# Optimization experiments

Hardware: AMD Instinct MI355X
Metric: run time of the kernel (lower is better)

Reference implementation:

```python
import jax, jax.numpy as jnp
import numpy as np

B, S, D, H = 4, 2048, 1024, 16
DK = D // H
NEG = -1e9


def setup_inputs() -> dict:
    key = jax.random.key(0)
    k1, k2, k3, k4 = jax.random.split(key, 4)
    x = jax.random.normal(k1, (B, S, D), dtype=jnp.float32)
    # seq_lens sorted descending; first entry must equal max_len (as the torch
    # code uses seq_lens[0] as max_len for the mask)
    sl = jax.random.randint(k2, (B,), S // 2, S + 1)
    sl = jnp.sort(sl)[::-1].at[0].set(S).astype(jnp.int64)
    # params of the output projection nn.Linear(d_m, d_m)
    lim = 1.0 / np.sqrt(D)
    W = jax.random.uniform(k3, (D, D), minval=-lim, maxval=lim, dtype=jnp.float32)
    b = jax.random.uniform(k4, (D,), minval=-lim, maxval=lim, dtype=jnp.float32)
    return {"x": x, "seq_lens": sl, "W": W, "b": b}


def reference(x, seq_lens, W, b):
    # key padding mask: (B, 1, 1, S) -> True where key position is valid
    valid = jnp.arange(S)[None, :] < seq_lens[:, None]          # (B, S)
    mask = valid[:, None, None, :]                              # (B, 1, 1, S)
    # split heads: (B, S, D) -> (B, H, S, DK)
    xh = x.reshape(B, S, H, DK).transpose(0, 2, 1, 3)
    scores = jnp.einsum("bhqd,bhkd->bhqk", xh, xh) / jnp.sqrt(jnp.float32(DK))
    scores = jnp.where(mask, scores, NEG)
    attn = jax.nn.softmax(scores, axis=-1)                      # (B, H, S, S)
    # dropout(0.1) omitted (eval-mode deterministic reference)
    ctx = jnp.einsum("bhqk,bhkd->bhqd", attn, xh)
    ctx = ctx.transpose(0, 2, 1, 3).reshape(B, S, D)
    out = ctx @ W.T + b                                         # (B, S, D)
    return (jnp.sum(out, axis=1), attn)
```

## Files before the change

kernel.cpp:

```cpp
#include <hip/hip_runtime.h>

#define S_  2048
#define D_  1024
#define H_  16
#define B_  4
#define NT  32

typedef __attribute__((ext_vector_type(8))) short short8;
typedef __attribute__((ext_vector_type(4))) float f32x4;

__device__ __forceinline__ unsigned short f2bf(float f) {
  unsigned int u = __float_as_uint(f);
  u += 0x7fffu + ((u >> 16) & 1u);
  return (unsigned short)(u >> 16);
}
__device__ __forceinline__ unsigned int pack2(float a, float b) {
  return (unsigned int)f2bf(a) | ((unsigned int)f2bf(b) << 16);
}
__device__ __forceinline__ float h2f(unsigned int u, int shft) {
  unsigned short hs = (unsigned short)(u >> shft);
  return (float)__builtin_bit_cast(_Float16, hs);
}

#define SCL   0.18033688011112042f
#define EBIAS 12.0f

__global__ __launch_bounds__(256) void xcvt(const float* __restrict__ x,
                                            unsigned short* __restrict__ xh) {
  const int n = blockIdx.x;
  const int bh = n >> 5, chunk = n & 31;
  const int b = bh >> 4, h = bh & 15;
  const int r = threadIdx.x >> 2, cg = threadIdx.x & 3;
  const int srow = chunk * 64 + r;
  const float* src = x + ((size_t)b * S_ + srow) * D_ + h * 64 + cg * 16;
  float4 v0 = ((const float4*)src)[0];
  float4 v1 = ((const float4*)src)[1];
  float4 v2 = ((const float4*)src)[2];
  float4 v3 = ((const float4*)src)[3];
  uint4 w0, w1;
  w0.x = pack2(v0.x, v0.y); w0.y = pack2(v0.z, v0.w);
  w0.z = pack2(v1.x, v1.y); w0.w = pack2(v1.z, v1.w);
  w1.x = pack2(v2.x, v2.y); w1.y = pack2(v2.z, v2.w);
  w1.z = pack2(v3.x, v3.y); w1.w = pack2(v3.z, v3.w);
  unsigned short* dst = xh + ((size_t)bh * S_ + srow) * 64 + cg * 16;
  *(uint4*)dst = w0;
  *(uint4*)(dst + 8) = w1;
}

__global__ __launch_bounds__(768, 1) void attn_fused(
    const unsigned short* __restrict__ xh, const int* __restrict__ sl32,
    float* __restrict__ attn, unsigned int* __restrict__ cpart)
{
  __shared__ __align__(16) unsigned int ebuf[2][8][2048];
  __shared__ float wbuf[128];
  __shared__ float invbuf[2][16];

  const int n    = blockIdx.x;
  const int xcd  = n & 7;
  const int j    = n >> 3;
  const int bh   = (j >> 2) * 8 + xcd;
  const int q0   = (j & 3) * NT;
  const int b    = bh >> 4;
  const int tid  = threadIdx.x;
  const int wv   = tid >> 6;
  const bool is_comp = wv < 8;
  const int lane = tid & 63;
  const int lo   = lane & 15;
  const int g    = lane >> 4;

  const bool is64 = (sl32[1] == 0);
  const int seqlen = is64 ? sl32[2 * b] : sl32[b];

  const unsigned short* xk = xh + (size_t)bh * S_ * 64;

  const int sA = ((g * 2) & 6) << 2;
  const int wt  = tid & 255;
  const int wr  = wt >> 4, wc = wt & 15;
  const int r2w = wr >> 1, shw = (wr & 1) * 16, sw2 = (r2w & 6) << 2;

  for (int ti = 0; ti <= NT; ++ti) {
    unsigned int (*eb)[2048] = ebuf[ti & 1];
    const unsigned int (*ebp)[2048] = ebuf[(ti + 1) & 1];

    if (is_comp) {
      if (ti < NT) {
        const int qt = q0 + ti;
        short8 aq0 = *(const short8*)(xk + (size_t)(qt * 16 + lo) * 64 + g * 8);
        short8 aq1 = *(const short8*)(xk + (size_t)(qt * 16 + lo) * 64 + g * 8 + 32);
        float r0 = 0.f, r1 = 0.f, r2s = 0.f, r3 = 0.f;
#pragma unroll 4
        for (int c = 0; c < 16; ++c) {
          const int kt = c * 8 + wv;
          const int kg = kt * 16 + lo;
          const unsigned short* kp = xk + (size_t)kg * 64 + g * 8;
          short8 b0 = *(const short8*)kp;
          short8 b1 = *(const short8*)(kp + 32);
          f32x4 acc = {0.f, 0.f, 0.f, 0.f};
          acc = __builtin_amdgcn_mfma_f32_16x16x32_bf16(aq0, b0, acc, 0, 0, 0);
          acc = __builtin_amdgcn_mfma_f32_16x16x32_bf16(aq1, b1, acc, 0, 0, 0);
          const bool valid = kg < seqlen;
          float e0 = valid ? exp2f(acc[0] * SCL - EBIAS) : 0.f;
          float e1 = valid ? exp2f(acc[1] * SCL - EBIAS) : 0.f;
          float e2 = valid ? exp2f(acc[2] * SCL - EBIAS) : 0.f;
          float e3 = valid ? exp2f(acc[3] * SCL - EBIAS) : 0.f;
          r0 += e0; r1 += e1; r2s += e2; r3 += e3;
          eb[g * 2][kg ^ sA] =
              __builtin_bit_cast(unsigned int, __builtin_amdgcn_cvt_pkrtz(e0, e1));
          eb[g * 2 + 1][kg ^ sA] =
              __builtin_bit_cast(unsigned int, __builtin_amdgcn_cvt_pkrtz(e2, e3));
        }
        float rs[4] = {r0, r1, r2s, r3};
#pragma unroll
        for (int r4 = 0; r4 < 4; ++r4) {
          float v = rs[r4];
          v += __shfl_xor(v, 1);
          v += __shfl_xor(v, 2);
          v += __shfl_xor(v, 4);
          v += __shfl_xor(v, 8);
          if (lo == 0) wbuf[wv * 16 + g * 4 + r4] = v;
        }
      }
    } else if (ti > 0) {
      const float* ivp = invbuf[(ti - 1) & 1];
      const float vr = ivp[wr];
      float* prow = attn + (size_t)bh * S_ * S_ +
                    (size_t)((q0 + ti - 1) * 16 + wr) * S_;
#pragma unroll 8
      for (int i = 0; i < 32; ++i) {
        const int k0 = wc * 4 + i * 64;
        uint4 u = *(const uint4*)&ebp[r2w][k0 ^ sw2];
        f32x4 v = {h2f(u.x, shw) * vr, h2f(u.y, shw) * vr,
                   h2f(u.z, shw) * vr, h2f(u.w, shw) * vr};
        __builtin_nontemporal_store(v, (f32x4*)(prow + k0));
      }
      const int c0 = wt * 8;
      float a0 = 0.f, a1 = 0.f, a2 = 0.f, a3 = 0.f;
      float a4 = 0.f, a5 = 0.f, a6 = 0.f, a7 = 0.f;
#pragma unroll
      for (int r2 = 0; r2 < 8; ++r2) {
        const int s = (r2 & 6) << 2;
        const uint4 uA = *(const uint4*)&ebp[r2][c0 ^ s];
        const uint4 uB = *(const uint4*)&ebp[r2][(c0 ^ s) + 4];
        const float i0 = ivp[2 * r2], i1 = ivp[2 * r2 + 1];
        a0 += h2f(uA.x, 0) * i0 + h2f(uA.x, 16) * i1;
        a1 += h2f(uA.y, 0) * i0 + h2f(uA.y, 16) * i1;
        a2 += h2f(uA.z, 0) * i0 + h2f(uA.z, 16) * i1;
        a3 += h2f(uA.w, 0) * i0 + h2f(uA.w, 16) * i1;
        a4 += h2f(uB.x, 0) * i0 + h2f(uB.x, 16) * i1;
        a5 += h2f(uB.y, 0) * i0 + h2f(uB.y, 16) * i1;
        a6 += h2f(uB.z, 0) * i0 + h2f(uB.z, 16) * i1;
        a7 += h2f(uB.w, 0) * i0 + h2f(uB.w, 16) * i1;
      }
      uint4 w;
      w.x = __builtin_bit_cast(unsigned int, __builtin_amdgcn_cvt_pkrtz(a0, a1));
      w.y = __builtin_bit_cast(unsigned int, __builtin_amdgcn_cvt_pkrtz(a2, a3));
      w.z = __builtin_bit_cast(unsigned int, __builtin_amdgcn_cvt_pkrtz(a4, a5));
      w.w = __builtin_bit_cast(unsigned int, __builtin_amdgcn_cvt_pkrtz(a6, a7));
      *(uint4*)&cpart[(size_t)(bh * 128 + q0 + ti - 1) * 1024 + wt * 4] = w;
    }

    __syncthreads();
    if (ti < NT && tid < 16) {
      float s = 0.f;
#pragma unroll
      for (int w8 = 0; w8 < 8; ++w8) s += wbuf[w8 * 16 + tid];
      invbuf[ti & 1][tid] = 1.0f / s;
    }
    __syncthreads();
  }
}

__global__ __launch_bounds__(256) void csum2(const unsigned int* __restrict__ cpart,
                                             const unsigned short* __restrict__ xh,
                                             float* __restrict__ csump) {
  __shared__ float csh[256];
  __shared__ float part[4][64];
  const int bh = blockIdx.x >> 3, oct = blockIdx.x & 7;
  const int t = threadIdx.x;
  {
    const int k = oct * 256 + t;
    const unsigned short* cp =
        (const unsigned short*)cpart + (size_t)bh * 128 * 2048 + k;
    float s = 0.f;
#pragma unroll 8
    for (int q = 0; q < 128; ++q)
      s += (float)__builtin_bit_cast(_Float16, cp[(size_t)q * 2048]);
    csh[t] = s;
  }
  __syncthreads();
  const int seg = t >> 6, d = t & 63;
  const unsigned short* xb = xh + (size_t)bh * S_ * 64 + d;
  const int k0 = oct * 256 + seg * 64;
  float acc = 0.f;
#pragma unroll 4
  for (int kk = 0; kk < 64; ++kk) {
    float xv = __uint_as_float((unsigned int)xb[(size_t)(k0 + kk) * 64] << 16);
    acc += csh[seg * 64 + kk] * xv;
  }
  part[seg][d] = acc;
  __syncthreads();
  if (t < 64)
    csump[((size_t)oct * 64 + bh) * 64 + d] =
        part[0][d] + part[1][d] + part[2][d] + part[3][d];
}

__global__ __launch_bounds__(256) void proj_k(const float* __restrict__ csump,
                                              const float* __restrict__ W,
                                              const float* __restrict__ bias,
                                              float* __restrict__ out0) {
  const int idx = blockIdx.x * 4 + (threadIdx.x >> 6);
  const int b = idx >> 10, d = idx & 1023;
  const int lane = threadIdx.x & 63;
  const float* wr = W + (size_t)d * D_;
  float acc = 0.f;
#pragma unroll
  for (int e = 0; e < 16; ++e) {
    const int ei = lane + e * 64;
    const int bhh = b * 16 + (ei >> 6);
    const int dd = ei & 63;
    float cv = 0.f;
#pragma unroll
    for (int oct = 0; oct < 8; ++oct)
      cv += csump[((size_t)oct * 64 + bhh) * 64 + dd];
    acc += cv * wr[ei];
  }
  acc += __shfl_xor(acc, 32);
  acc += __shfl_xor(acc, 16);
  acc += __shfl_xor(acc, 8);
  acc += __shfl_xor(acc, 4);
  acc += __shfl_xor(acc, 2);
  acc += __shfl_xor(acc, 1);
  if (lane == 0) out0[idx] = acc + 2048.0f * bias[d];
}

extern "C" void kernel_launch(void* const* d_in, const int* in_sizes, int n_in,
                              void* d_out, int out_size, void* d_ws, size_t ws_size,
                              hipStream_t stream) {
  const float* x    = (const float*)d_in[0];
  const int*   sl   = (const int*)d_in[1];
  const float* W    = (const float*)d_in[2];
  const float* bias = (const float*)d_in[3];

  float* out0 = (float*)d_out;
  float* attn = out0 + B_ * D_;

  unsigned int* cpart = (unsigned int*)d_ws;
  float* csump = (float*)(cpart + (size_t)64 * 128 * 1024);
  unsigned short* xh = (unsigned short*)(csump + 8 * 64 * 64);

  hipLaunchKernelGGL(xcvt,       dim3(2048), dim3(256), 0, stream, x, xh);
  hipLaunchKernelGGL(attn_fused, dim3(256),  dim3(768), 0, stream, xh, sl, attn, cpart);
  hipLaunchKernelGGL(csum2,      dim3(512),  dim3(256), 0, stream, cpart, xh, csump);
  hipLaunchKernelGGL(proj_k,     dim3(1024), dim3(256), 0, stream, csump, W, bias, out0);
}
```

Baseline: 352.7 us.

## Merge compute and writer warp roles into unified 512-thread interleaved loop

The fused attention kernel drops its split of 8 compute waves plus 4 writer waves and uses 8 waves that each do both jobs. In the same loop, each wave interleaves the MFMA/exp work for the current query tile with the normalized attn stores for the previous tile. The column-partial reduction now runs right after the inverse sums are ready, reading the current buffer rather than waiting a step. Barriers are replaced by an explicit lgkmcnt wait plus s_barrier. The aim is to spread the large attn store stream across more waves and let it overlap with compute, at the cost of heavier per-wave register and instruction pressure.

```diff
diff --git a/kernel.cpp b/kernel.cpp
--- a/kernel.cpp
+++ b/kernel.cpp
@@ -20,6 +20,11 @@
 __device__ __forceinline__ float h2f(unsigned int u, int shft) {
   unsigned short hs = (unsigned short)(u >> shft);
   return (float)__builtin_bit_cast(_Float16, hs);
+}
+
+__device__ __forceinline__ void bar_lgkm() {
+  asm volatile("s_waitcnt lgkmcnt(0)" ::: "memory");
+  __builtin_amdgcn_s_barrier();
 }
 
 #define SCL   0.18033688011112042f
@@ -47,7 +52,7 @@
   *(uint4*)(dst + 8) = w1;
 }
 
-__global__ __launch_bounds__(768, 1) void attn_fused(
+__global__ __launch_bounds__(512, 1) void attn_fused(
     const unsigned short* __restrict__ xh, const int* __restrict__ sl32,
     float* __restrict__ attn, unsigned int* __restrict__ cpart)
 {
@@ -63,7 +68,6 @@
   const int b    = bh >> 4;
   const int tid  = threadIdx.x;
   const int wv   = tid >> 6;
-  const bool is_comp = wv < 8;
   const int lane = tid & 63;
   const int lo   = lane & 15;
   const int g    = lane >> 4;
@@ -74,99 +78,97 @@
   const unsigned short* xk = xh + (size_t)bh * S_ * 64;
 
   const int sA = ((g * 2) & 6) << 2;
-  const int wt  = tid & 255;
-  const int wr  = wt >> 4, wc = wt & 15;
-  const int r2w = wr >> 1, shw = (wr & 1) * 16, sw2 = (r2w & 6) << 2;
+  const int row_w = tid >> 5;
+  const int cu    = tid & 31;
+  const int r2w = row_w >> 1, shw = (row_w & 1) * 16, sw2 = (r2w & 6) << 2;
+  const int c0 = tid * 4;
 
   for (int ti = 0; ti <= NT; ++ti) {
     unsigned int (*eb)[2048] = ebuf[ti & 1];
     const unsigned int (*ebp)[2048] = ebuf[(ti + 1) & 1];
-
-    if (is_comp) {
-      if (ti < NT) {
-        const int qt = q0 + ti;
-        short8 aq0 = *(const short8*)(xk + (size_t)(qt * 16 + lo) * 64 + g * 8);
-        short8 aq1 = *(const short8*)(xk + (size_t)(qt * 16 + lo) * 64 + g * 8 + 32);
-        float r0 = 0.f, r1 = 0.f, r2s = 0.f, r3 = 0.f;
-#pragma unroll 4
-        for (int c = 0; c < 16; ++c) {
-          const int kt = c * 8 + wv;
-          const int kg = kt * 16 + lo;
-          const unsigned short* kp = xk + (size_t)kg * 64 + g * 8;
-          short8 b0 = *(const short8*)kp;
-          short8 b1 = *(const short8*)(kp + 32);
-          f32x4 acc = {0.f, 0.f, 0.f, 0.f};
-          acc = __builtin_amdgcn_mfma_f32_16x16x32_bf16(aq0, b0, acc, 0, 0, 0);
-          acc = __builtin_amdgcn_mfma_f32_16x16x32_bf16(aq1, b1, acc, 0, 0, 0);
-          const bool valid = kg < seqlen;
-          float e0 = valid ? exp2f(acc[0] * SCL - EBIAS) : 0.f;
-          float e1 = valid ? exp2f(acc[1] * SCL - EBIAS) : 0.f;
-          float e2 = valid ? exp2f(acc[2] * SCL - EBIAS) : 0.f;
-          float e3 = valid ? exp2f(acc[3] * SCL - EBIAS) : 0.f;
-          r0 += e0; r1 += e1; r2s += e2; r3 += e3;
-          eb[g * 2][kg ^ sA] =
-              __builtin_bit_cast(unsigned int, __builtin_amdgcn_cvt_pkrtz(e0, e1));
-          eb[g * 2 + 1][kg ^ sA] =
-              __builtin_bit_cast(unsigned int, __builtin_amdgcn_cvt_pkrtz(e2, e3));
-        }
-        float rs[4] = {r0, r1, r2s, r3};
-#pragma unroll
-        for (int r4 = 0; r4 < 4; ++r4) {
-          float v = rs[r4];
-          v += __shfl_xor(v, 1);
-          v += __shfl_xor(v, 2);
-          v += __shfl_xor(v, 4);
-          v += __shfl_xor(v, 8);
-          if (lo == 0) wbuf[wv * 16 + g * 4 + r4] = v;
-        }
-      }
-    } else if (ti > 0) {
-      const float* ivp = invbuf[(ti - 1) & 1];
-      const float vr = ivp[wr];
-      float* prow = attn + (size_t)bh * S_ * S_ +
-                    (size_t)((q0 + ti - 1) * 16 + wr) * S_;
-#pragma unroll 8
-      for (int i = 0; i < 32; ++i) {
-        const int k0 = wc * 4 + i * 64;
-        uint4 u = *(const uint4*)&ebp[r2w][k0 ^ sw2];
+    const bool has_c = ti < NT;
+    const bool has_w = ti > 0;
+
+    short8 aq0 = {}, aq1 = {};
+    if (has_c) {
+      const int qt = q0 + ti;
+      aq0 = *(const short8*)(xk + (size_t)(qt * 16 + lo) * 64 + g * 8);
+      aq1 = *(const short8*)(xk + (size_t)(qt * 16 + lo) * 64 + g * 8 + 32);
+    }
+    float r0 = 0.f, r1 = 0.f, r2s = 0.f, r3 = 0.f;
+    const float vr = has_w ? invbuf[(ti + 1) & 1][row_w] : 0.f;
+    float* prow = attn + (size_t)bh * S_ * S_ +
+                  (size_t)((q0 + ti - 1) * 16 + row_w) * S_;
+
+#pragma unroll
+    for (int i = 0; i < 16; ++i) {
+      if (has_c) {
+        const int kt = i * 8 + wv;
+        const int kg = kt * 16 + lo;
+        const unsigned short* kp = xk + (size_t)kg * 64 + g * 8;
+        short8 b0 = *(const short8*)kp;
+        short8 b1 = *(const short8*)(kp + 32);
+        f32x4 acc = {0.f, 0.f, 0.f, 0.f};
+        acc = __builtin_amdgcn_mfma_f32_16x16x32_bf16(aq0, b0, acc, 0, 0, 0);
+        acc = __builtin_amdgcn_mfma_f32_16x16x32_bf16(aq1, b1, acc, 0, 0, 0);
+        const bool valid = kg < seqlen;
+        float e0 = valid ? exp2f(acc[0] * SCL - EBIAS) : 0.f;
+        float e1 = valid ? exp2f(acc[1] * SCL - EBIAS) : 0.f;
+        float e2 = valid ? exp2f(acc[2] * SCL - EBIAS) : 0.f;
+        float e3 = valid ? exp2f(acc[3] * SCL - EBIAS) : 0.f;
+        r0 += e0; r1 += e1; r2s += e2; r3 += e3;
+        eb[g * 2][kg ^ sA] =
+            __builtin_bit_cast(unsigned int, __builtin_amdgcn_cvt_pkrtz(e0, e1));
+        eb[g * 2 + 1][kg ^ sA] =
+            __builtin_bit_cast(unsigned int, __builtin_amdgcn_cvt_pkrtz(e2, e3));
+      }
+      if (has_w) {
+        const int col0 = i * 128 + cu * 4;
+        uint4 u = *(const uint4*)&ebp[r2w][col0 ^ sw2];
         f32x4 v = {h2f(u.x, shw) * vr, h2f(u.y, shw) * vr,
                    h2f(u.z, shw) * vr, h2f(u.w, shw) * vr};
-        __builtin_nontemporal_store(v, (f32x4*)(prow + k0));
-      }
-      const int c0 = wt * 8;
+        __builtin_nontemporal_store(v, (f32x4*)(prow + col0));
+      }
+    }
+
+    if (has_c) {
+      float rs[4] = {r0, r1, r2s, r3};
+#pragma unroll
+      for (int r4 = 0; r4 < 4; ++r4) {
+        float v = rs[r4];
+        v += __shfl_xor(v, 1);
+        v += __shfl_xor(v, 2);
+        v += __shfl_xor(v, 4);
+        v += __shfl_xor(v, 8);
+        if (lo == 0) wbuf[wv * 16 + g * 4 + r4] = v;
+      }
+    }
+    bar_lgkm();
+    if (has_c && tid < 16) {
+      float s = 0.f;
+#pragma unroll
+      for (int w8 = 0; w8 < 8; ++w8) s += wbuf[w8 * 16 + tid];
+      invbuf[ti & 1][tid] = 1.0f / s;
+    }
+    bar_lgkm();
+    if (has_c) {
+      const float* ivc = invbuf[ti & 1];
       float a0 = 0.f, a1 = 0.f, a2 = 0.f, a3 = 0.f;
-      float a4 = 0.f, a5 = 0.f, a6 = 0.f, a7 = 0.f;
 #pragma unroll
       for (int r2 = 0; r2 < 8; ++r2) {
         const int s = (r2 & 6) << 2;
-        const uint4 uA = *(const uint4*)&ebp[r2][c0 ^ s];
-        const uint4 uB = *(const uint4*)&ebp[r2][(c0 ^ s) + 4];
-        const float i0 = ivp[2 * r2], i1 = ivp[2 * r2 + 1];
-        a0 += h2f(uA.x, 0) * i0 + h2f(uA.x, 16) * i1;
-        a1 += h2f(uA.y, 0) * i0 + h2f(uA.y, 16) * i1;
-        a2 += h2f(uA.z, 0) * i0 + h2f(uA.z, 16) * i1;
-        a3 += h2f(uA.w, 0) * i0 + h2f(uA.w, 16) * i1;
-        a4 += h2f(uB.x, 0) * i0 + h2f(uB.x, 16) * i1;
-        a5 += h2f(uB.y, 0) * i0 + h2f(uB.y, 16) * i1;
-        a6 += h2f(uB.z, 0) * i0 + h2f(uB.z, 16) * i1;
-        a7 += h2f(uB.w, 0) * i0 + h2f(uB.w, 16) * i1;
-      }
-      uint4 w;
+        const uint4 u = *(const uint4*)&eb[r2][c0 ^ s];
+        const float i0 = ivc[2 * r2], i1 = ivc[2 * r2 + 1];
+        a0 += h2f(u.x, 0) * i0 + h2f(u.x, 16) * i1;
+        a1 += h2f(u.y, 0) * i0 + h2f(u.y, 16) * i1;
+        a2 += h2f(u.z, 0) * i0 + h2f(u.z, 16) * i1;
+        a3 += h2f(u.w, 0) * i0 + h2f(u.w, 16) * i1;
+      }
+      uint2 w;
       w.x = __builtin_bit_cast(unsigned int, __builtin_amdgcn_cvt_pkrtz(a0, a1));
       w.y = __builtin_bit_cast(unsigned int, __builtin_amdgcn_cvt_pkrtz(a2, a3));
-      w.z = __builtin_bit_cast(unsigned int, __builtin_amdgcn_cvt_pkrtz(a4, a5));
-      w.w = __builtin_bit_cast(unsigned int, __builtin_amdgcn_cvt_pkrtz(a6, a7));
-      *(uint4*)&cpart[(size_t)(bh * 128 + q0 + ti - 1) * 1024 + wt * 4] = w;
-    }
-
-    __syncthreads();
-    if (ti < NT && tid < 16) {
-      float s = 0.f;
-#pragma unroll
-      for (int w8 = 0; w8 < 8; ++w8) s += wbuf[w8 * 16 + tid];
-      invbuf[ti & 1][tid] = 1.0f / s;
-    }
-    __syncthreads();
+      *(uint2*)&cpart[(size_t)(bh * 128 + q0 + ti) * 1024 + tid * 2] = w;
+    }
   }
 }
 
@@ -249,7 +251,7 @@
   unsigned short* xh = (unsigned short*)(csump + 8 * 64 * 64);
 
   hipLaunchKernelGGL(xcvt,       dim3(2048), dim3(256), 0, stream, x, xh);
-  hipLaunchKernelGGL(attn_fused, dim3(256),  dim3(768), 0, stream, xh, sl, attn, cpart);
+  hipLaunchKernelGGL(attn_fused, dim3(256),  dim3(512), 0, stream, xh, sl, attn, cpart);
   hipLaunchKernelGGL(csum2,      dim3(512),  dim3(256), 0, stream, cpart, xh, csump);
   hipLaunchKernelGGL(proj_k,     dim3(1024), dim3(256), 0, stream, csump, W, bias, out0);
 }
```

New measurement: 369.1 us. 1.05x slower.
